# Kernel tuning notes

Hardware: AMD Instinct MI355X
Metric: run time of the kernel (lower is better)

## Reference

```python
import jax, jax.numpy as jnp
import numpy as np

NUM_NODES_G1 = 60000
NUM_NODES_G2 = 50000
NUM_REL = 16
NUM_BASES = 4
DIM = 128  # node_dim == hidden_dim == final_dim
L_COMMON = 100


def _concept_layer(x, edge_index):
    # Gather-based concept propagation: x_i <- x_i + mean_{j in N(i)} x_j
    src, dst = edge_index[0], edge_index[1]
    n = x.shape[0]
    agg = jax.ops.segment_sum(x[src], dst, num_segments=n)
    deg = jax.ops.segment_sum(jnp.ones((src.shape[0],), x.dtype), dst, num_segments=n)
    return x + agg / jnp.clip(deg, 1.0)[:, None]


def _rgcn_layer(x, edge_index, edge_type, basis, comp, root, bias):
    # Basis-decomposed RGCN: out_i = x_i @ root + bias + sum_r (1/|N_i^r|) sum_{j in N_i^r} x_j @ W_r,
    # W_r = sum_b comp[r,b] * basis[b]. Reorder: scatter comp-weighted x[src] per basis, then one GEMM per basis.
    src, dst = edge_index[0], edge_index[1]
    n = x.shape[0]
    e = src.shape[0]
    seg = dst * NUM_REL + edge_type  # per-(node, relation) bucket
    cnt = jax.ops.segment_sum(jnp.ones((e,), x.dtype), seg, num_segments=n * NUM_REL)
    norm = 1.0 / jnp.clip(cnt, 1.0)
    coef = comp[edge_type] * norm[seg][:, None]  # [E, B]
    xsrc = x[src]  # [E, D] -- dominant gather traffic
    out = x @ root + bias
    for b in range(NUM_BASES):  # small fixed loop over bases
        agg_b = jax.ops.segment_sum(xsrc * coef[:, b:b + 1], dst, num_segments=n)
        out = out + agg_b @ basis[b]
    return out


def setup_inputs() -> dict:
    key = jax.random.key(0)
    ks = jax.random.split(key, 16)
    e2, e1 = 800000, 800000
    return {
        "edge_index_g2": jax.random.randint(ks[0], (2, e2), 0, NUM_NODES_G2),
        "edge_type_g2": jax.random.randint(ks[1], (e2,), 0, NUM_REL),
        "edge_index_g1": jax.random.randint(ks[2], (2, e1), 0, NUM_NODES_G1),
        "left_common": jax.random.randint(ks[3], (L_COMMON,), 0, NUM_NODES_G1),
        "all_node_embedding": jax.random.normal(ks[4], (NUM_NODES_G1, DIM), jnp.float32),
        "basis1": jax.random.normal(ks[5], (NUM_BASES, DIM, DIM), jnp.float32) * 0.05,
        "comp1": jax.random.normal(ks[6], (NUM_REL, NUM_BASES), jnp.float32),
        "root1": jax.random.normal(ks[7], (DIM, DIM), jnp.float32) * 0.05,
        "bias1": jnp.zeros((DIM,), jnp.float32),
        "basis2": jax.random.normal(ks[8], (NUM_BASES, DIM, DIM), jnp.float32) * 0.05,
        "comp2": jax.random.normal(ks[9], (NUM_REL, NUM_BASES), jnp.float32),
        "root2": jax.random.normal(ks[10], (DIM, DIM), jnp.float32) * 0.05,
        "bias2": jnp.zeros((DIM,), jnp.float32),
        "weights": jax.random.uniform(ks[11], (DIM, 1), jnp.float32),
    }


def reference(edge_index_g2, edge_type_g2, edge_index_g1, left_common,
              all_node_embedding, basis1, comp1, root1, bias1,
              basis2, comp2, root2, bias2, weights):
    x_g1 = jax.nn.relu(_concept_layer(all_node_embedding, edge_index_g1))
    x = x_g1[:NUM_NODES_G2]
    x = _rgcn_layer(x, edge_index_g2, edge_type_g2, basis1, comp1, root1, bias1)
    x = jax.nn.relu(x)  # relu_use == 1
    x_g2 = _rgcn_layer(x, edge_index_g2, edge_type_g2, basis2, comp2, root2, bias2)
    ty = x_g1[left_common]  # [L, D]
    # mul_def outer elementwise product followed by matmul with weights collapses to one contraction:
    # logits[n,l] = sum_d x_g2[n,d] * ty[l,d] * w[d]
    logits = jnp.einsum('nd,ld,d->nl', x_g2, ty, weights[:, 0])
    return jax.nn.softmax(logits, axis=1)
```

## Files before the change

kernel.cpp:

```cpp
#include <hip/hip_runtime.h>
#include <hip/hip_bf16.h>
#include <math.h>

#define N1 60000
#define N2 50000
#define DIM 128
#define NREL 16
#define NB 4
#define LCOM 100
#define LPAD 112
#define NPART 8
#define NC 16

typedef __attribute__((ext_vector_type(8))) short short8;
typedef __attribute__((ext_vector_type(4))) float f32x4;
typedef __attribute__((ext_vector_type(4))) _Float16 half4;
typedef __attribute__((ext_vector_type(8))) _Float16 half8;

__device__ __forceinline__ float bf2f(unsigned short u) {
    union { unsigned int i; float f; } c; c.i = ((unsigned int)u) << 16; return c.f;
}
__device__ __forceinline__ unsigned short f2bf(float f) {
    union { float f; unsigned int i; } c; c.f = f;
    unsigned int r = c.i + 0x7FFF + ((c.i >> 16) & 1);
    return (unsigned short)(r >> 16);
}
__device__ __forceinline__ void split8(float4 a, float4 b, short8& h, short8& l) {
    float f[8] = {a.x, a.y, a.z, a.w, b.x, b.y, b.z, b.w};
#pragma unroll
    for (int j = 0; j < 8; j++) {
        unsigned short hh = f2bf(f[j]);
        h[j] = (short)hh;
        l[j] = (short)f2bf(f[j] - bf2f(hh));
    }
}

__global__ __launch_bounds__(256) void k_prelude(
        const int* __restrict__ ei1, int E1, int* __restrict__ degs1,
        const int* __restrict__ ei2, int E2, int* __restrict__ degs2,
        const float* __restrict__ root1, const float* __restrict__ basis1,
        unsigned short* __restrict__ Wh1, unsigned short* __restrict__ Wl1,
        const float* __restrict__ root2, const float* __restrict__ basis2,
        unsigned short* __restrict__ Wh2, unsigned short* __restrict__ Wl2, int PB,
        const float* __restrict__ emb, _Float16* __restrict__ embh, int n4) {
    __shared__ int hist[7500];
    int b = blockIdx.x;
    const int HB = NPART * NC;
    if (b < 2 * HB) {
        int isg2 = b >= HB;
        int bb = isg2 ? b - HB : b;
        int p = bb & (NPART - 1);
        int c = bb >> 3;
        const int* dsts = isg2 ? ei2 + E2 : ei1 + E1;
        int E = isg2 ? E2 : E1;
        int N = isg2 ? N2 : N1;
        int* degs = isg2 ? degs2 : degs1;
        const int W = (N + NPART - 1) / NPART;
        int lo = p * W, hi = min(lo + W, N);
        int span = hi - lo;
        for (int i = threadIdx.x; i < span; i += 256) hist[i] = 0;
        __syncthreads();
        int chunk = (E + NC - 1) / NC;
        int e0 = c * chunk, e1 = min(e0 + chunk, E);
        for (int base = e0; base < e1; base += 1024) {
            int d[4]; bool ok[4];
#pragma unroll
            for (int j = 0; j < 4; j++) {
                int e = base + threadIdx.x + j * 256;
                bool inb = e < e1;
                d[j] = inb ? __builtin_nontemporal_load(dsts + e) : -1;
                ok[j] = inb && d[j] >= lo && d[j] < hi;
            }
#pragma unroll
            for (int j = 0; j < 4; j++)
                if (ok[j]) atomicAdd(&hist[d[j] - lo], 1);
        }
        __syncthreads();
        int* slice = degs + (size_t)c * N + lo;
        for (int i = threadIdx.x; i < span; i += 256) slice[i] = hist[i];
    } else if (b < 2 * HB + PB) {
        int t = (b - 2 * HB) * 256 + threadIdx.x;
        if (t < 2 * 640 * 128) {
            int which = t >= 640 * 128;
            int tt = which ? t - 640 * 128 : t;
            const float* root = which ? root2 : root1;
            const float* basis = which ? basis2 : basis1;
            unsigned short* Wh = which ? Wh2 : Wh1;
            unsigned short* Wl = which ? Wl2 : Wl1;
            int k = tt >> 7, n = tt & 127;
            float v = (k < 128) ? root[k * 128 + n] : basis[(k - 128) * 128 + n];
            unsigned short h = f2bf(v);
            Wh[n * 640 + k] = h;
            Wl[n * 640 + k] = f2bf(v - bf2f(h));
        }
    } else {
        int i = (b - 2 * HB - PB) * 256 + threadIdx.x;
        if (i < n4) {
            float4 v = ((const float4*)emb)[i];
            half4 o = {(_Float16)v.x, (_Float16)v.y, (_Float16)v.z, (_Float16)v.w};
            ((half4*)embh)[i] = o;
        }
    }
}

__global__ __launch_bounds__(256) void k_scan_p1m(const int* __restrict__ degsA, int* __restrict__ degA,
                                                  int nA, int nbA, int* __restrict__ bsumA,
                                                  const int* __restrict__ degsB, int* __restrict__ degB,
                                                  int nB, int* __restrict__ bsumB) {
    __shared__ int red[256];
    const int* degs; int* deg; int n; int* bsum; int b;
    if ((int)blockIdx.x < nbA) { degs = degsA; deg = degA; n = nA; bsum = bsumA; b = blockIdx.x; }
    else { degs = degsB; deg = degB; n = nB; bsum = bsumB; b = blockIdx.x - nbA; }
    int base = b * 1024;
    int tid = threadIdx.x;
    int s = 0;
#pragma unroll
    for (int j = 0; j < 4; j++) {
        int i = base + tid * 4 + j;
        if (i < n) {
            int v = 0;
#pragma unroll
            for (int c = 0; c < NC; c++) v += degs[(size_t)c * n + i];
            deg[i] = v;
            s += v;
        }
    }
    red[tid] = s;
    __syncthreads();
    for (int d = 128; d; d >>= 1) {
        if (tid < d) red[tid] += red[tid + d];
        __syncthreads();
    }
    if (tid == 0) bsum[b] = red[0];
}

__global__ __launch_bounds__(64) void k_scan_p2m(const int* __restrict__ bsumA, int* __restrict__ boffA,
                                                 int* __restrict__ offA, int nbA, int nA,
                                                 const int* __restrict__ bsumB, int* __restrict__ boffB,
                                                 int* __restrict__ offB, int nbB, int nB) {
    __shared__ int s[64];
    const int* bsum; int* boff; int* off; int nb; int n;
    if (blockIdx.x == 0) { bsum = bsumA; boff = boffA; off = offA; nb = nbA; n = nA; }
    else { bsum = bsumB; boff = boffB; off = offB; nb = nbB; n = nB; }
    int tid = threadIdx.x;
    int v = (tid < nb) ? bsum[tid] : 0;
    s[tid] = v;
    __syncthreads();
    for (int d = 1; d < 64; d <<= 1) {
        int t = (tid >= d) ? s[tid - d] : 0;
        __syncthreads();
        s[tid] += t;
        __syncthreads();
    }
    if (tid < nb) boff[tid] = s[tid] - v;
    if (tid == 63) off[n] = s[63];
}

__global__ __launch_bounds__(256) void k_scan_p3m(const int* __restrict__ inA, const int* __restrict__ boffA,
                                                  int* __restrict__ offA, int* __restrict__ curA,
                                                  int nA, int nbA,
                                                  const int* __restrict__ inB, const int* __restrict__ boffB,
                                                  int* __restrict__ offB, int* __restrict__ curB, int nB) {
    __shared__ int red[256];
    const int* in; const int* boff; int* off; int* cur; int n; int b;
    if ((int)blockIdx.x < nbA) { in = inA; boff = boffA; off = offA; cur = curA; n = nA; b = blockIdx.x; }
    else { in = inB; boff = boffB; off = offB; cur = curB; n = nB; b = blockIdx.x - nbA; }
    int base = b * 1024;
    int tid = threadIdx.x;
    int v[4];
    int s = 0;
#pragma unroll
    for (int j = 0; j < 4; j++) {
        int i = base + tid * 4 + j;
        v[j] = (i < n) ? in[i] : 0;
        s += v[j];
    }
    red[tid] = s;
    __syncthreads();
    for (int d = 1; d < 256; d <<= 1) {
        int t = (tid >= d) ? red[tid - d] : 0;
        __syncthreads();
        red[tid] += t;
        __syncthreads();
    }
    int run = boff[b] + red[tid] - s;
#pragma unroll
    for (int j = 0; j < 4; j++) {
        int i = base + tid * 4 + j;
        if (i < n) {
            off[i] = run; cur[i] = run;
            run += v[j];
        }
    }
}

__global__ __launch_bounds__(256) void k_scat(const int* __restrict__ ei1, int E1,
                                              int* __restrict__ cur1, int* __restrict__ elist1, int G1) {
    int p = blockIdx.x & (NPART - 1);
    int c = blockIdx.x >> 3;
    const int W = (N1 + NPART - 1) / NPART;
    int lo = p * W, hi = min(lo + W, N1);
    int chunk = (E1 + G1 - 1) / G1;
    int e0 = c * chunk, e1 = min(e0 + chunk, E1);
    for (int base = e0; base < e1; base += 1024) {
        int d[4], s[4]; bool ok[4];
#pragma unroll
        for (int j = 0; j < 4; j++) {
            int e = base + threadIdx.x + j * 256;
            bool inb = e < e1;
            d[j] = inb ? __builtin_nontemporal_load(ei1 + E1 + e) : -1;
            s[j] = inb ? __builtin_nontemporal_load(ei1 + e) : 0;
            ok[j] = inb && d[j] >= lo && d[j] < hi;
        }
#pragma unroll
        for (int j = 0; j < 4; j++) {
            if (ok[j]) {
                int pos = atomicAdd(cur1 + d[j], 1);
                elist1[pos] = s[j];
            }
        }
    }
}

__global__ __launch_bounds__(256) void k_mix(
        const _Float16* __restrict__ embh, const float* __restrict__ emb,
        const int* __restrict__ off1, const int* __restrict__ elist1,
        float* __restrict__ xg1, _Float16* __restrict__ xg1h, int CONC_B,
        const int* __restrict__ ei2, const int* __restrict__ et2, int E2,
        int* __restrict__ cur2, int* __restrict__ elist2, int G2,
        const int* __restrict__ lc, const float* __restrict__ w,
        unsigned short* __restrict__ tyh, unsigned short* __restrict__ tyl) {
    int b = blockIdx.x;
    int SC2B = NPART * G2;
    if (b < SC2B) {
        int p = b & (NPART - 1);
        int c = b >> 3;
        const int W = (N2 + NPART - 1) / NPART;
        int lo = p * W, hi = min(lo + W, N2);
        int chunk = (E2 + G2 - 1) / G2;
        int e0 = c * chunk, e1 = min(e0 + chunk, E2);
        for (int base = e0; base < e1; base += 1024) {
            int d[4], s[4], t[4]; bool ok[4];
#pragma unroll
            for (int j = 0; j < 4; j++) {
                int e = base + threadIdx.x + j * 256;
                bool inb = e < e1;
                d[j] = inb ? __builtin_nontemporal_load(ei2 + E2 + e) : -1;
                s[j] = inb ? __builtin_nontemporal_load(ei2 + e) : 0;
                t[j] = inb ? __builtin_nontemporal_load(et2 + e) : 0;
                ok[j] = inb && d[j] >= lo && d[j] < hi;
            }
#pragma unroll
            for (int j = 0; j < 4; j++) {
                if (ok[j]) {
                    int pos = atomicAdd(cur2 + d[j], 1);
                    elist2[pos] = (s[j] << 4) | t[j];
                }
            }
        }
    } else if (b < SC2B + CONC_B) {
        int node = (b - SC2B) * 4 + (threadIdx.x >> 6);
        int lane = threadIdx.x & 63;
        if (node >= N2) return;
        int quad = lane >> 4, d8 = (lane & 15) * 8;
        int s0 = off1[node], s1 = off1[node + 1];
        float acc[8] = {};
        int i = s0;
        for (; i + 8 <= s1; i += 8) {
            int sa = elist1[i + quad];
            int sb = elist1[i + 4 + quad];
            half8 ha = *(const half8*)(embh + (size_t)sa * DIM + d8);
            half8 hb = *(const half8*)(embh + (size_t)sb * DIM + d8);
#pragma unroll
            for (int j = 0; j < 8; j++) acc[j] += (float)ha[j] + (float)hb[j];
        }
        if (i + 4 <= s1) {
            int sa = elist1[i + quad];
            half8 ha = *(const half8*)(embh + (size_t)sa * DIM + d8);
#pragma unroll
            for (int j = 0; j < 8; j++) acc[j] += (float)ha[j];
            i += 4;
        }
        if (i < s1) {
            int e = i + quad;
            bool ok = e < s1;
            int s = elist1[ok ? e : i];
            half8 hv = *(const half8*)(embh + (size_t)s * DIM + d8);
            if (ok) {
#pragma unroll
                for (int j = 0; j < 8; j++) acc[j] += (float)hv[j];
            }
        }
#pragma unroll
        for (int j = 0; j < 8; j++) {
            acc[j] += __shfl_xor(acc[j], 16, 64);
            acc[j] += __shfl_xor(acc[j], 32, 64);
        }
        if (quad == 0) {
            float inv = 1.0f / (float)max(s1 - s0, 1);
            const float* ep = emb + (size_t)node * DIM + d8;
            float4 e0 = *(const float4*)(ep);
            float4 e1 = *(const float4*)(ep + 4);
            float o[8];
            o[0] = fmaxf(e0.x + acc[0] * inv, 0.f);
            o[1] = fmaxf(e0.y + acc[1] * inv, 0.f);
            o[2] = fmaxf(e0.z + acc[2] * inv, 0.f);
            o[3] = fmaxf(e0.w + acc[3] * inv, 0.f);
            o[4] = fmaxf(e1.x + acc[4] * inv, 0.f);
            o[5] = fmaxf(e1.y + acc[5] * inv, 0.f);
            o[6] = fmaxf(e1.z + acc[6] * inv, 0.f);
            o[7] = fmaxf(e1.w + acc[7] * inv, 0.f);
            float4 w0 = {o[0], o[1], o[2], o[3]};
            float4 w1 = {o[4], o[5], o[6], o[7]};
            *(float4*)(xg1 + (size_t)node * DIM + d8) = w0;
            *(float4*)(xg1 + (size_t)node * DIM + d8 + 4) = w1;
            half8 oh;
#pragma unroll
            for (int j = 0; j < 8; j++) oh[j] = (_Float16)o[j];
            *(half8*)(xg1h + (size_t)node * DIM + d8) = oh;
        }
    } else {
        if (threadIdx.x >= 64) return;
        int l = b - SC2B - CONC_B;
        int lane = threadIdx.x;
        int d0 = lane * 2;
        if (l >= LCOM) {
            ushort2 z = {0, 0};
            *(ushort2*)(tyh + (size_t)l * 128 + d0) = z;
            *(ushort2*)(tyl + (size_t)l * 128 + d0) = z;
            return;
        }
        int row = lc[l];
        int s0 = off1[row], s1 = off1[row + 1];
        float2 acc = {0.f, 0.f};
        for (int i = s0; i < s1; i++) {
            int s = elist1[i];
            float2 v = *(const float2*)(emb + (size_t)s * DIM + lane * 2);
            acc.x += v.x; acc.y += v.y;
        }
        float inv = 1.0f / (float)max(s1 - s0, 1);
        float2 e = *(const float2*)(emb + (size_t)row * DIM + lane * 2);
        float v0 = fmaxf(e.x + acc.x * inv, 0.f) * w[d0];
        float v1 = fmaxf(e.y + acc.y * inv, 0.f) * w[d0 + 1];
        unsigned short h0 = f2bf(v0), h1 = f2bf(v1);
        ushort2 hh = {h0, h1};
        ushort2 ll = {f2bf(v0 - bf2f(h0)), f2bf(v1 - bf2f(h1))};
        *(ushort2*)(tyh + (size_t)l * 128 + d0) = hh;
        *(ushort2*)(tyl + (size_t)l * 128 + d0) = ll;
    }
}

__global__ __launch_bounds__(256) void k_rgcn_gather(const _Float16* __restrict__ xh,
                                                     const int* __restrict__ off,
                                                     const int* __restrict__ elist,
                                                     const float* __restrict__ comp,
                                                     float* __restrict__ agg, int n) {
    __shared__ float scomp[NREL * NB];
    __shared__ float nrmlds[4][NREL];
    if (threadIdx.x < NREL * NB) scomp[threadIdx.x] = comp[threadIdx.x];
    __syncthreads();
    int nb = threadIdx.x >> 6;
    int node = blockIdx.x * 4 + nb;
    int lane = threadIdx.x & 63;
    if (node >= n) return;
    int s0 = off[node], s1 = off[node + 1];
    unsigned long long c0 = 0, c1 = 0;
    for (int i = s0 + lane; i < s1; i += 64) {
        int t = elist[i] & 15;
        if (t < 8) c0 += 1ull << (8 * t); else c1 += 1ull << (8 * (t - 8));
    }
#pragma unroll
    for (int o = 32; o; o >>= 1) {
        c0 += __shfl_xor(c0, o, 64);
        c1 += __shfl_xor(c1, o, 64);
    }
    if (lane < NREL) {
        unsigned int c = (lane < 8) ? (unsigned int)((c0 >> (8 * lane)) & 255)
                                    : (unsigned int)((c1 >> (8 * (lane - 8))) & 255);
        nrmlds[nb][lane] = 1.0f / (float)max(c, 1u);
    }
    int quad = lane >> 4, d8 = (lane & 15) * 8;
    float a[4][8] = {};
#define RGE(P, GATE)                                                           \
    {                                                                          \
        int s_ = (P) >> 4, t_ = (P) & 15;                                      \
        float nr_ = nrmlds[nb][t_] * (GATE);                                   \
        float4 cf_ = *(const float4*)(scomp + t_ * 4);                         \
        half8 hv_ = *(const half8*)(xh + (size_t)s_ * DIM + d8);               \
        float c0_ = cf_.x * nr_, c1_ = cf_.y * nr_;                            \
        float c2_ = cf_.z * nr_, c3_ = cf_.w * nr_;                            \
        _Pragma("unroll")                                                      \
        for (int j = 0; j < 8; j++) {                                          \
            float v_ = (float)hv_[j];                                          \
            a[0][j] = fmaf(c0_, v_, a[0][j]);                                  \
            a[1][j] = fmaf(c1_, v_, a[1][j]);                                  \
            a[2][j] = fmaf(c2_, v_, a[2][j]);                                  \
            a[3][j] = fmaf(c3_, v_, a[3][j]);                                  \
        }                                                                      \
    }
    int i = s0;
    for (; i + 8 <= s1; i += 8) {
        int pa = elist[i + quad];
        int pb = elist[i + 4 + quad];
        RGE(pa, 1.0f);
        RGE(pb, 1.0f);
    }
    if (i + 4 <= s1) {
        int pa = elist[i + quad];
        RGE(pa, 1.0f);
        i += 4;
    }
    if (i < s1) {
        int e = i + quad;
        bool ok = e < s1;
        int pa = elist[ok ? e : i];
        RGE(pa, ok ? 1.0f : 0.0f);
    }
#undef RGE
#pragma unroll
    for (int bb = 0; bb < 4; bb++)
#pragma unroll
        for (int j = 0; j < 8; j++) {
            a[bb][j] += __shfl_xor(a[bb][j], 16, 64);
            a[bb][j] += __shfl_xor(a[bb][j], 32, 64);
        }
    if (quad == 0) {
        float* o = agg + (size_t)node * (NB * DIM) + d8;
#pragma unroll
        for (int bb = 0; bb < 4; bb++) {
            float4 v0 = {a[bb][0], a[bb][1], a[bb][2], a[bb][3]};
            float4 v1 = {a[bb][4], a[bb][5], a[bb][6], a[bb][7]};
            *(float4*)(o + bb * DIM) = v0;
            *(float4*)(o + bb * DIM + 4) = v1;
        }
    }
}

#define LDSK 40
__global__ __launch_bounds__(256) void k_gemm(const float* __restrict__ x,
                                              const float* __restrict__ agg,
                                              const unsigned short* __restrict__ Wh,
                                              const unsigned short* __restrict__ Wl,
                                              const float* __restrict__ bias,
                                              float* __restrict__ out,
                                              _Float16* __restrict__ out_h, int relu) {
    __shared__ __align__(16) short Ah[128 * LDSK];
    __shared__ __align__(16) short Al[128 * LDSK];
    __shared__ __align__(16) short Bh[128 * LDSK];
    __shared__ __align__(16) short Bl[128 * LDSK];
    int tid = threadIdx.x;
    int lane = tid & 63, wid = tid >> 6;
    int wave_m = wid >> 1, wave_n = wid & 1;
    int l15 = lane & 15, quad = lane >> 4;
    int row0 = blockIdx.x * 128;

    int srow = tid >> 1, skh = (tid & 1) * 16;

    f32x4 acc[4][4] = {};
    for (int k0 = 0; k0 < 640; k0 += 32) {
        {
            int rg = row0 + srow;
            float4 q0 = {0, 0, 0, 0}, q1 = q0, q2 = q0, q3 = q0;
            if (rg < N2) {
                const float* src = (k0 < 128) ? (x + (size_t)rg * 128 + k0 + skh)
                                              : (agg + (size_t)rg * 512 + (k0 - 128) + skh);
                q0 = *(const float4*)(src + 0);
                q1 = *(const float4*)(src + 4);
                q2 = *(const float4*)(src + 8);
                q3 = *(const float4*)(src + 12);
            }
            short8 h0, l0, h1, l1;
            split8(q0, q1, h0, l0);
            split8(q2, q3, h1, l1);
            *(short8*)(&Ah[srow * LDSK + skh]) = h0;
            *(short8*)(&Ah[srow * LDSK + skh + 8]) = h1;
            *(short8*)(&Al[srow * LDSK + skh]) = l0;
            *(short8*)(&Al[srow * LDSK + skh + 8]) = l1;
        }
        {
            const unsigned short* sh = Wh + (size_t)srow * 640 + k0 + skh;
            const unsigned short* sl = Wl + (size_t)srow * 640 + k0 + skh;
            *(short8*)(&Bh[srow * LDSK + skh]) = *(const short8*)(sh);
            *(short8*)(&Bh[srow * LDSK + skh + 8]) = *(const short8*)(sh + 8);
            *(short8*)(&Bl[srow * LDSK + skh]) = *(const short8*)(sl);
            *(short8*)(&Bl[srow * LDSK + skh + 8]) = *(const short8*)(sl + 8);
        }
        __syncthreads();
        short8 ah[4], al[4], bh[4], bl[4];
#pragma unroll
        for (int i = 0; i < 4; i++) {
            int ro = (wave_m * 64 + i * 16 + l15) * LDSK + quad * 8;
            ah[i] = *(const short8*)(&Ah[ro]);
            al[i] = *(const short8*)(&Al[ro]);
        }
#pragma unroll
        for (int j = 0; j < 4; j++) {
            int ro = (wave_n * 64 + j * 16 + l15) * LDSK + quad * 8;
            bh[j] = *(const short8*)(&Bh[ro]);
            bl[j] = *(const short8*)(&Bl[ro]);
        }
#pragma unroll
        for (int i = 0; i < 4; i++)
#pragma unroll
            for (int j = 0; j < 4; j++) {
                acc[i][j] = __builtin_amdgcn_mfma_f32_16x16x32_bf16(al[i], bh[j], acc[i][j], 0, 0, 0);
                acc[i][j] = __builtin_amdgcn_mfma_f32_16x16x32_bf16(ah[i], bl[j], acc[i][j], 0, 0, 0);
                acc[i][j] = __builtin_amdgcn_mfma_f32_16x16x32_bf16(ah[i], bh[j], acc[i][j], 0, 0, 0);
            }
        __syncthreads();
    }
#pragma unroll
    for (int j = 0; j < 4; j++) {
        int gcol = wave_n * 64 + j * 16 + l15;
        float bv = bias[gcol];
#pragma unroll
        for (int i = 0; i < 4; i++) {
            int grow_base = row0 + wave_m * 64 + i * 16 + quad * 4;
#pragma unroll
            for (int r = 0; r < 4; r++) {
                int grow = grow_base + r;
                if (grow >= N2) continue;
                float v = acc[i][j][r] + bv;
                if (relu) v = fmaxf(v, 0.f);
                out[(size_t)grow * 128 + gcol] = v;
                if (out_h) out_h[(size_t)grow * 128 + gcol] = (_Float16)v;
            }
        }
    }
}

__global__ __launch_bounds__(256) void k_logits(const float* __restrict__ h2,
                                                const unsigned short* __restrict__ tyh,
                                                const unsigned short* __restrict__ tyl,
                                                float* __restrict__ out, int M) {
    int wid = threadIdx.x >> 6, lane = threadIdx.x & 63;
    int l15 = lane & 15, quad = lane >> 4;
    int row0w = blockIdx.x * 64 + wid * 16;
    int arow = min(row0w + l15, M - 1);
    f32x4 acc[7] = {};
#pragma unroll
    for (int k0 = 0; k0 < 128; k0 += 32) {
        const float* ap = h2 + (size_t)arow * 128 + k0 + quad * 8;
        float4 q0 = *(const float4*)(ap);
        float4 q1 = *(const float4*)(ap + 4);
        short8 ah, al;
        split8(q0, q1, ah, al);
#pragma unroll
        for (int j = 0; j < 7; j++) {
            size_t bo = (size_t)(j * 16 + l15) * 128 + k0 + quad * 8;
            short8 bh = *(const short8*)(tyh + bo);
            short8 bl = *(const short8*)(tyl + bo);
            acc[j] = __builtin_amdgcn_mfma_f32_16x16x32_bf16(al, bh, acc[j], 0, 0, 0);
            acc[j] = __builtin_amdgcn_mfma_f32_16x16x32_bf16(ah, bl, acc[j], 0, 0, 0);
            acc[j] = __builtin_amdgcn_mfma_f32_16x16x32_bf16(ah, bh, acc[j], 0, 0, 0);
        }
    }
    bool v6 = (l15 < LCOM - 96);
#pragma unroll
    for (int r = 0; r < 4; r++) {
        int grow = row0w + quad * 4 + r;
        float m = -INFINITY;
#pragma unroll
        for (int j = 0; j < 6; j++) m = fmaxf(m, acc[j][r]);
        if (v6) m = fmaxf(m, acc[6][r]);
        m = fmaxf(m, __shfl_xor(m, 8, 64));
        m = fmaxf(m, __shfl_xor(m, 4, 64));
        m = fmaxf(m, __shfl_xor(m, 2, 64));
        m = fmaxf(m, __shfl_xor(m, 1, 64));
        float e[7];
        float s = 0.f;
#pragma unroll
        for (int j = 0; j < 6; j++) { e[j] = __expf(acc[j][r] - m); s += e[j]; }
        e[6] = v6 ? __expf(acc[6][r] - m) : 0.f;
        s += e[6];
        s += __shfl_xor(s, 8, 64);
        s += __shfl_xor(s, 4, 64);
        s += __shfl_xor(s, 2, 64);
        s += __shfl_xor(s, 1, 64);
        float inv = 1.0f / s;
        if (grow < M) {
#pragma unroll
            for (int j = 0; j < 6; j++) out[(size_t)grow * LCOM + j * 16 + l15] = e[j] * inv;
            if (v6) out[(size_t)grow * LCOM + 96 + l15] = e[6] * inv;
        }
    }
}

extern "C" void kernel_launch(void* const* d_in, const int* in_sizes, int n_in,
                              void* d_out, int out_size, void* d_ws, size_t ws_size,
                              hipStream_t stream) {
    const int* ei2 = (const int*)d_in[0];
    const int* et2 = (const int*)d_in[1];
    const int* ei1 = (const int*)d_in[2];
    const int* lc = (const int*)d_in[3];
    const float* emb = (const float*)d_in[4];
    const float* basis1 = (const float*)d_in[5];
    const float* comp1 = (const float*)d_in[6];
    const float* root1 = (const float*)d_in[7];
    const float* bias1 = (const float*)d_in[8];
    const float* basis2 = (const float*)d_in[9];
    const float* comp2 = (const float*)d_in[10];
    const float* root2 = (const float*)d_in[11];
    const float* bias2 = (const float*)d_in[12];
    const float* wts = (const float*)d_in[13];
    float* out = (float*)d_out;
    int E2 = in_sizes[0] / 2, E1 = in_sizes[2] / 2;

    float* ws = (float*)d_ws;
    float* xg1 = ws;
    float* h1 = xg1 + 6400000;
    float* agg = h1 + 6400000;
    _Float16* emb_h = (_Float16*)(agg + 25600000);
    unsigned short* tyh = (unsigned short*)(emb_h + 7680000);
    unsigned short* tyl = tyh + LPAD * 128;
    unsigned short* Wh1 = tyl + LPAD * 128;
    unsigned short* Wl1 = Wh1 + 81920;
    unsigned short* Wh2 = Wl1 + 81920;
    unsigned short* Wl2 = Wh2 + 81920;
    int* ipool = (int*)(Wl2 + 81920);
    int* deg1 = ipool;
    int* deg2 = deg1 + 60000;
    int* off1 = deg2 + 50000;
    int* cur1 = off1 + 60001;
    int* elist1 = cur1 + 60000;
    int* off2 = elist1 + 800000;
    int* cur2 = off2 + 50001;
    int* elist2 = cur2 + 50000;
    int* bsum1 = elist2 + 800000;
    int* boff1 = bsum1 + 64;
    int* bsum2 = boff1 + 64;
    int* boff2 = bsum2 + 64;
    int* degs1 = (int*)agg;
    int* degs2 = degs1 + NC * N1;
    _Float16* xg1_h = (_Float16*)h1;
    _Float16* h1_h = emb_h;
    float* h2 = xg1;

    const int NB1 = (N1 + 1023) / 1024;
    const int NB2 = (N2 + 1023) / 1024;
    const int PB = (2 * 640 * 128) / 256;
    const int CB = (N1 * DIM / 4 + 255) / 256;
    const int CONC_B = (N2 + 3) / 4;
    const int G1 = 128, G2 = 128;
    const int SC2B = NPART * G2;

    k_prelude<<<2 * NPART * NC + PB + CB, 256, 0, stream>>>(
        ei1, E1, degs1, ei2, E2, degs2,
        root1, basis1, Wh1, Wl1, root2, basis2, Wh2, Wl2, PB,
        emb, emb_h, N1 * DIM / 4);

    k_scan_p1m<<<NB1 + NB2, 256, 0, stream>>>(degs1, deg1, N1, NB1, bsum1,
                                              degs2, deg2, N2, bsum2);
    k_scan_p2m<<<2, 64, 0, stream>>>(bsum1, boff1, off1, NB1, N1, bsum2, boff2, off2, NB2, N2);
    k_scan_p3m<<<NB1 + NB2, 256, 0, stream>>>(deg1, boff1, off1, cur1, N1, NB1,
                                              deg2, boff2, off2, cur2, N2);

    k_scat<<<NPART * G1, 256, 0, stream>>>(ei1, E1, cur1, elist1, G1);

    k_mix<<<SC2B + CONC_B + LPAD, 256, 0, stream>>>(
        emb_h, emb, off1, elist1, xg1, xg1_h, CONC_B,
        ei2, et2, E2, cur2, elist2, G2,
        lc, wts, tyh, tyl);

    k_rgcn_gather<<<CONC_B, 256, 0, stream>>>(xg1_h, off2, elist2, comp1, agg, N2);
    k_gemm<<<(N2 + 127) / 128, 256, 0, stream>>>(xg1, agg, Wh1, Wl1, bias1, h1, h1_h, 1);

    k_rgcn_gather<<<CONC_B, 256, 0, stream>>>(h1_h, off2, elist2, comp2, agg, N2);
    k_gemm<<<(N2 + 127) / 128, 256, 0, stream>>>(h1, agg, Wh2, Wl2, bias2, h2, (_Float16*)nullptr, 0);

    k_logits<<<(N2 + 63) / 64, 256, 0, stream>>>(h2, tyh, tyl, out, N2);
}
```

Baseline: 532.2 us.

## Replace global atomic CSR fill with per-chunk offsets and LDS atomics

The per-chunk degree histograms from the prelude are turned into exclusive per-chunk start offsets inside the scan kernel. The scatter kernel then places each edge using an LDS atomic counter per destination plus the precomputed chunk offset, so it no longer issues global atomics on a cursor array. Both graphs are now scattered in one launch, and the G2 scatter is pulled out of the mix kernel. The cost is a larger count buffer (NC raised to 64), a strided per-node loop over 64 chunks in the scan, and a serial dependency from scan to scatter to mix for G2.

```diff
diff --git a/kernel.cpp b/kernel.cpp
--- a/kernel.cpp
+++ b/kernel.cpp
@@ -10,7 +10,7 @@
 #define LCOM 100
 #define LPAD 112
 #define NPART 8
-#define NC 16
+#define NC 64
 
 typedef __attribute__((ext_vector_type(8))) short short8;
 typedef __attribute__((ext_vector_type(4))) float f32x4;
@@ -116,10 +116,9 @@
     int s = 0;
 #pragma unroll
     for (int j = 0; j < 4; j++) {
-        int i = base + tid * 4 + j;
+        int i = base + tid + j * 256;
         if (i < n) {
             int v = 0;
-#pragma unroll
             for (int c = 0; c < NC; c++) v += degs[(size_t)c * n + i];
             deg[i] = v;
             s += v;
@@ -157,14 +156,14 @@
 }
 
 __global__ __launch_bounds__(256) void k_scan_p3m(const int* __restrict__ inA, const int* __restrict__ boffA,
-                                                  int* __restrict__ offA, int* __restrict__ curA,
+                                                  int* __restrict__ offA, int* __restrict__ sbA,
                                                   int nA, int nbA,
                                                   const int* __restrict__ inB, const int* __restrict__ boffB,
-                                                  int* __restrict__ offB, int* __restrict__ curB, int nB) {
+                                                  int* __restrict__ offB, int* __restrict__ sbB, int nB) {
     __shared__ int red[256];
-    const int* in; const int* boff; int* off; int* cur; int n; int b;
-    if ((int)blockIdx.x < nbA) { in = inA; boff = boffA; off = offA; cur = curA; n = nA; b = blockIdx.x; }
-    else { in = inB; boff = boffB; off = offB; cur = curB; n = nB; b = blockIdx.x - nbA; }
+    const int* in; const int* boff; int* off; int* sb; int n; int b;
+    if ((int)blockIdx.x < nbA) { in = inA; boff = boffA; off = offA; sb = sbA; n = nA; b = blockIdx.x; }
+    else { in = inB; boff = boffB; off = offB; sb = sbB; n = nB; b = blockIdx.x - nbA; }
     int base = b * 1024;
     int tid = threadIdx.x;
     int v[4];
@@ -188,35 +187,63 @@
     for (int j = 0; j < 4; j++) {
         int i = base + tid * 4 + j;
         if (i < n) {
-            off[i] = run; cur[i] = run;
+            off[i] = run;
             run += v[j];
         }
     }
+    __syncthreads();
+    for (int i = base + tid; i < min(base + 1024, n); i += 256) {
+        int run2 = off[i];
+        for (int c = 0; c < NC; c++) {
+            size_t idx = (size_t)c * n + i;
+            int t = sb[idx];
+            sb[idx] = run2;
+            run2 += t;
+        }
+    }
 }
 
 __global__ __launch_bounds__(256) void k_scat(const int* __restrict__ ei1, int E1,
-                                              int* __restrict__ cur1, int* __restrict__ elist1, int G1) {
-    int p = blockIdx.x & (NPART - 1);
-    int c = blockIdx.x >> 3;
-    const int W = (N1 + NPART - 1) / NPART;
-    int lo = p * W, hi = min(lo + W, N1);
-    int chunk = (E1 + G1 - 1) / G1;
-    int e0 = c * chunk, e1 = min(e0 + chunk, E1);
+                                              const int* __restrict__ sb1, int* __restrict__ elist1,
+                                              const int* __restrict__ ei2, const int* __restrict__ et2,
+                                              int E2, const int* __restrict__ sb2, int* __restrict__ elist2) {
+    __shared__ int lcur[7500];
+    int b = blockIdx.x;
+    const int HB = NPART * NC;
+    int isg2 = b >= HB;
+    int bb = isg2 ? b - HB : b;
+    int p = bb & (NPART - 1);
+    int c = bb >> 3;
+    const int* ei = isg2 ? ei2 : ei1;
+    int E = isg2 ? E2 : E1;
+    int N = isg2 ? N2 : N1;
+    const int* sb = isg2 ? sb2 : sb1;
+    int* elist = isg2 ? elist2 : elist1;
+    const int W = (N + NPART - 1) / NPART;
+    int lo = p * W, hi = min(lo + W, N);
+    int span = hi - lo;
+    for (int i = threadIdx.x; i < span; i += 256) lcur[i] = 0;
+    __syncthreads();
+    const int* sbc = sb + (size_t)c * N;
+    int chunk = (E + NC - 1) / NC;
+    int e0 = c * chunk, e1 = min(e0 + chunk, E);
     for (int base = e0; base < e1; base += 1024) {
-        int d[4], s[4]; bool ok[4];
+        int d[4], sv[4], tv[4]; bool ok[4];
 #pragma unroll
         for (int j = 0; j < 4; j++) {
             int e = base + threadIdx.x + j * 256;
             bool inb = e < e1;
-            d[j] = inb ? __builtin_nontemporal_load(ei1 + E1 + e) : -1;
-            s[j] = inb ? __builtin_nontemporal_load(ei1 + e) : 0;
+            d[j] = inb ? __builtin_nontemporal_load(ei + E + e) : -1;
+            sv[j] = inb ? __builtin_nontemporal_load(ei + e) : 0;
+            tv[j] = (inb && isg2) ? __builtin_nontemporal_load(et2 + e) : 0;
             ok[j] = inb && d[j] >= lo && d[j] < hi;
         }
 #pragma unroll
         for (int j = 0; j < 4; j++) {
             if (ok[j]) {
-                int pos = atomicAdd(cur1 + d[j], 1);
-                elist1[pos] = s[j];
+                int li = atomicAdd(&lcur[d[j] - lo], 1);
+                int pay = isg2 ? ((sv[j] << 4) | tv[j]) : sv[j];
+                elist[sbc[d[j]] + li] = pay;
             }
         }
     }
@@ -226,40 +253,11 @@
         const _Float16* __restrict__ embh, const float* __restrict__ emb,
         const int* __restrict__ off1, const int* __restrict__ elist1,
         float* __restrict__ xg1, _Float16* __restrict__ xg1h, int CONC_B,
-        const int* __restrict__ ei2, const int* __restrict__ et2, int E2,
-        int* __restrict__ cur2, int* __restrict__ elist2, int G2,
         const int* __restrict__ lc, const float* __restrict__ w,
         unsigned short* __restrict__ tyh, unsigned short* __restrict__ tyl) {
     int b = blockIdx.x;
-    int SC2B = NPART * G2;
-    if (b < SC2B) {
-        int p = b & (NPART - 1);
-        int c = b >> 3;
-        const int W = (N2 + NPART - 1) / NPART;
-        int lo = p * W, hi = min(lo + W, N2);
-        int chunk = (E2 + G2 - 1) / G2;
-        int e0 = c * chunk, e1 = min(e0 + chunk, E2);
-        for (int base = e0; base < e1; base += 1024) {
-            int d[4], s[4], t[4]; bool ok[4];
-#pragma unroll
-            for (int j = 0; j < 4; j++) {
-                int e = base + threadIdx.x + j * 256;
-                bool inb = e < e1;
-                d[j] = inb ? __builtin_nontemporal_load(ei2 + E2 + e) : -1;
-                s[j] = inb ? __builtin_nontemporal_load(ei2 + e) : 0;
-                t[j] = inb ? __builtin_nontemporal_load(et2 + e) : 0;
-                ok[j] = inb && d[j] >= lo && d[j] < hi;
-            }
-#pragma unroll
-            for (int j = 0; j < 4; j++) {
-                if (ok[j]) {
-                    int pos = atomicAdd(cur2 + d[j], 1);
-                    elist2[pos] = (s[j] << 4) | t[j];
-                }
-            }
-        }
-    } else if (b < SC2B + CONC_B) {
-        int node = (b - SC2B) * 4 + (threadIdx.x >> 6);
+    if (b < CONC_B) {
+        int node = b * 4 + (threadIdx.x >> 6);
         int lane = threadIdx.x & 63;
         if (node >= N2) return;
         int quad = lane >> 4, d8 = (lane & 15) * 8;
@@ -321,7 +319,7 @@
         }
     } else {
         if (threadIdx.x >= 64) return;
-        int l = b - SC2B - CONC_B;
+        int l = b - CONC_B;
         int lane = threadIdx.x;
         int d0 = lane * 2;
         if (l >= LCOM) {
@@ -621,11 +619,9 @@
     int* deg1 = ipool;
     int* deg2 = deg1 + 60000;
     int* off1 = deg2 + 50000;
-    int* cur1 = off1 + 60001;
-    int* elist1 = cur1 + 60000;
+    int* elist1 = off1 + 60001;
     int* off2 = elist1 + 800000;
-    int* cur2 = off2 + 50001;
-    int* elist2 = cur2 + 50000;
+    int* elist2 = off2 + 50001;
     int* bsum1 = elist2 + 800000;
     int* boff1 = bsum1 + 64;
     int* bsum2 = boff1 + 64;
@@ -641,8 +637,6 @@
     const int PB = (2 * 640 * 128) / 256;
     const int CB = (N1 * DIM / 4 + 255) / 256;
     const int CONC_B = (N2 + 3) / 4;
-    const int G1 = 128, G2 = 128;
-    const int SC2B = NPART * G2;
 
     k_prelude<<<2 * NPART * NC + PB + CB, 256, 0, stream>>>(
         ei1, E1, degs1, ei2, E2, degs2,
@@ -652,14 +646,14 @@
     k_scan_p1m<<<NB1 + NB2, 256, 0, stream>>>(degs1, deg1, N1, NB1, bsum1,
                                               degs2, deg2, N2, bsum2);
     k_scan_p2m<<<2, 64, 0, stream>>>(bsum1, boff1, off1, NB1, N1, bsum2, boff2, off2, NB2, N2);
-    k_scan_p3m<<<NB1 + NB2, 256, 0, stream>>>(deg1, boff1, off1, cur1, N1, NB1,
-                                              deg2, boff2, off2, cur2, N2);
-
-    k_scat<<<NPART * G1, 256, 0, stream>>>(ei1, E1, cur1, elist1, G1);
-
-    k_mix<<<SC2B + CONC_B + LPAD, 256, 0, stream>>>(
+    k_scan_p3m<<<NB1 + NB2, 256, 0, stream>>>(deg1, boff1, off1, degs1, N1, NB1,
+                                              deg2, boff2, off2, degs2, N2);
+
+    k_scat<<<2 * NPART * NC, 256, 0, stream>>>(ei1, E1, degs1, elist1,
+                                               ei2, et2, E2, degs2, elist2);
+
+    k_mix<<<CONC_B + LPAD, 256, 0, stream>>>(
         emb_h, emb, off1, elist1, xg1, xg1_h, CONC_B,
-        ei2, et2, E2, cur2, elist2, G2,
         lc, wts, tyh, tyl);
 
     k_rgcn_gather<<<CONC_B, 256, 0, stream>>>(xg1_h, off2, elist2, comp1, agg, N2);
```

Measured after the change: 531.9 us. About the same (-0.1%).
